# Optimization experiments

Measured on AMD Instinct MI355X. Metric: run time of the kernel, lower is better.

Reference implementation:

```python
import jax, jax.numpy as jnp
import numpy as np

INPUT_DIM = 512
LATENT_DIM = 64
H1, H2 = 128, 64  # hardcoded hidden widths in Encoder/Decoder
BATCH = 4096


def _xavier(key, shape):
    fan_out, fan_in = shape
    std = jnp.sqrt(2.0 / (fan_in + fan_out))
    return std * jax.random.normal(key, shape, dtype=jnp.float32)


def setup_inputs() -> dict:
    key = jax.random.key(0)
    ks = jax.random.split(key, 10)
    d = LATENT_DIM
    n_pairs = d * (d - 1) // 2
    n_funcs = 1 + d + n_pairs  # bias + states + pairwise products
    inp = {
        "x": jax.random.normal(ks[0], (BATCH, INPUT_DIM), dtype=jnp.float32),
        "xdot": jax.random.normal(ks[1], (BATCH, INPUT_DIM), dtype=jnp.float32),
        # encoder weights (torch Linear layout: [out, in])
        "We1": _xavier(ks[2], (H1, INPUT_DIM)), "be1": jnp.zeros((H1,), jnp.float32),
        "We2": _xavier(ks[3], (H2, H1)),        "be2": jnp.zeros((H2,), jnp.float32),
        "We3": _xavier(ks[4], (d, H2)),         "be3": jnp.zeros((d,), jnp.float32),
        # decoder weights
        "Wd1": _xavier(ks[5], (H2, d)),         "bd1": jnp.zeros((H2,), jnp.float32),
        "Wd2": _xavier(ks[6], (H1, H2)),        "bd2": jnp.zeros((H1,), jnp.float32),
        "Wd3": _xavier(ks[7], (INPUT_DIM, H1)), "bd3": jnp.zeros((INPUT_DIM,), jnp.float32),
        "XI": jnp.ones((n_funcs, d), jnp.float32),
        "XI_mask": jnp.ones((n_funcs, d), jnp.float32),
    }
    return inp


def _mlp_with_jacobian(x, Ws, bs):
    """3-layer relu MLP; returns output and per-sample analytic Jacobian [B,out,in].
    Jacobian = diag(m3) W3 diag(m2) W2 diag(m1) W1 with relu masks m_l."""
    h = x
    J = None
    for W, b in zip(Ws, bs):
        h = h @ W.T + b                      # [B, out_l]
        m = (h > 0).astype(h.dtype)          # relu mask (grad 0 at 0, matching torch)
        h = jnp.maximum(h, 0)
        Wm = m[:, :, None] * W[None]         # [B, out_l, in_l]
        J = Wm if J is None else jnp.einsum('boh,bhi->boi', Wm, J)
    return h, J


def _sindy_library(z):
    B, d = z.shape
    iu, ju = np.triu_indices(d, k=1)
    ones = jnp.ones((B, 1), z.dtype)
    pairs = z[:, iu] * z[:, ju]              # [B, d(d-1)/2]
    return jnp.concatenate([ones, z, pairs], axis=1)


def reference(x, xdot, We1, be1, We2, be2, We3, be3,
              Wd1, bd1, Wd2, bd2, Wd3, bd3, XI, XI_mask):
    z, Jenc = _mlp_with_jacobian(x, (We1, We2, We3), (be1, be2, be3))
    dz_dt = jnp.einsum('bli,bi->bl', Jenc, xdot)
    xh, Jdec = _mlp_with_jacobian(z, (Wd1, Wd2, Wd3), (bd1, bd2, bd3))
    theta = _sindy_library(z)
    dz_dt_sindy = theta @ (XI_mask * XI)
    dxh_dt = jnp.einsum('bol,bl->bo', Jdec, dz_dt_sindy)
    return (xh, dxh_dt, z, dz_dt, dz_dt_sindy)
```

## Files before the change

kernel.cpp:

```cpp
#include <hip/hip_runtime.h>

#define BATCH 4096
#define IN_DIM 512
#define H1DIM 128
#define H2DIM 64
#define DDIM 64
#define NFUNC 2081
#define NFPAD 2112
#define CHUNK 704
#define KS_PER_CHUNK 22

typedef short bf16x8 __attribute__((ext_vector_type(8)));
typedef float f32x4 __attribute__((ext_vector_type(4)));
#define MFMA(a,b,c) __builtin_amdgcn_mfma_f32_16x16x32_bf16(a,b,c,0,0,0)

#define WSZ1 (H1DIM*IN_DIM)
#define WSZ2 (H2DIM*H1DIM)
#define WSZ3 (DDIM*H2DIM)
#define WSZ4 (H2DIM*DDIM)
#define WSZ5 (H1DIM*H2DIM)
#define WSZ6 (IN_DIM*H1DIM)

__device__ __forceinline__ short f2b(float f) {
    union { float f; unsigned u; } x; x.f = f;
    unsigned r = x.u + 0x7fffu + ((x.u >> 16) & 1u);
    return (short)(r >> 16);
}
__device__ __forceinline__ float b2f(short s) {
    union { unsigned u; float f; } x; x.u = ((unsigned)(unsigned short)s) << 16;
    return x.f;
}
__device__ __forceinline__ void split3f(float v, short& s0, short& s1, short& s2) {
    s0 = f2b(v); float r = v - b2f(s0);
    s1 = f2b(r); float r2 = r - b2f(s1);
    s2 = f2b(r2);
}
__device__ __forceinline__ uint2 pk4(const short* s) {
    union { short s[4]; uint2 u; } z;
    z.s[0] = s[0]; z.s[1] = s[1]; z.s[2] = s[2]; z.s[3] = s[3];
    return z.u;
}

template<int N> __device__ __forceinline__ void waitv() {
    asm volatile("s_waitcnt vmcnt(%0)" :: "n"(N) : "memory");
    __builtin_amdgcn_sched_barrier(0);
}

__device__ __forceinline__ void st_b16(short* t, int RS, int r, int c, short v) {
    int b = (c * 2) ^ ((r & 7) << 4);
    *(short*)((char*)(t + r * RS) + b) = v;
}
__device__ __forceinline__ void st_b64(short* t, int RS, int r, int c0, uint2 v) {
    int b = (c0 * 2) ^ ((r & 7) << 4);
    *(uint2*)((char*)(t + r * RS) + b) = v;
}
__device__ __forceinline__ bf16x8 ld_af(const short* t, int RS, int lane, int kbase) {
    int r = lane & 15;
    int b = ((kbase + (lane >> 4) * 8) * 2) ^ ((r & 7) << 4);
    return *(const bf16x8*)((const char*)(t + r * RS) + b);
}
__device__ __forceinline__ bf16x8 ld_bp(const short* P, int blk, int lane) {
    return *(const bf16x8*)(P + ((size_t)blk * 64 + lane) * 8);
}

__device__ __forceinline__ void mf9(bf16x8 f0, bf16x8 f1, bf16x8 f2, bf16x8 fv,
                                    bf16x8 b0, bf16x8 b1, bf16x8 b2,
                                    f32x4& P, f32x4& Q, f32x4& V) {
    P = MFMA(f0, b0, P); Q = MFMA(f1, b1, Q);
    P = MFMA(f1, b0, P); Q = MFMA(f0, b1, Q);
    P = MFMA(f2, b0, P); Q = MFMA(f2, b1, Q);
    P = MFMA(f0, b2, P); Q = MFMA(f1, b2, Q);
    V = MFMA(fv, b0, V);
}

__device__ __forceinline__ void epi_store(short* t0, short* t1, short* t2, short* tv, int RS,
                                          int lane, int col, const f32x4& P, const f32x4& Q,
                                          const f32x4& V, float bb)
{
    #pragma unroll
    for (int q = 0; q < 4; ++q) {
        int row = (lane >> 4) * 4 + q;
        float pre = P[q] + Q[q] + bb;
        float h = fmaxf(pre, 0.f);
        short s0, s1, s2;
        split3f(h, s0, s1, s2);
        st_b16(t0, RS, row, col, s0);
        st_b16(t1, RS, row, col, s1);
        st_b16(t2, RS, row, col, s2);
        st_b16(tv, RS, row, col, pre > 0.f ? f2b(V[q]) : (short)0);
    }
}

template<int K>
__device__ void pack_w(const float* __restrict__ W, short* __restrict__ dst, int NK,
                       int gid, int nthr)
{
    for (int i = gid; i < NK; i += nthr) {
        int c = i / K, k = i % K;
        int cb = c >> 4, ks = k >> 5;
        int L = (((k >> 3) & 3) << 4) | (c & 15);
        int j = k & 7;
        int idx = ((cb * (K / 32) + ks) * 64 + L) * 8 + j;
        short s0, s1, s2; split3f(W[i], s0, s1, s2);
        dst[idx] = s0; dst[idx + NK] = s1; dst[idx + 2 * NK] = s2;
    }
}

__global__ void initk(const float* __restrict__ x, const float* __restrict__ xdot,
                      const float* __restrict__ We1, const float* __restrict__ We2,
                      const float* __restrict__ We3, const float* __restrict__ Wd1,
                      const float* __restrict__ Wd2, const float* __restrict__ Wd3,
                      const float* __restrict__ XI, const float* __restrict__ XIm,
                      float* __restrict__ xh, float* __restrict__ dxh,
                      short* Wp1, short* Wp2, short* Wp3, short* Wp4, short* Wp5, short* Wp6,
                      short* xiP, int2* pk)
{
    int gid = blockIdx.x * blockDim.x + threadIdx.x;
    int nthr = gridDim.x * blockDim.x;

    for (int i = gid; i < (BATCH / 16) * 16 * 64; i += nthr) {
        int L = i & 63, ks = (i >> 6) & 15, rb = i >> 10;
        int row = rb * 16 + (L & 15);
        int k0 = ks * 32 + ((L >> 4) << 3);
        const float* px = &x[(size_t)row * IN_DIM + k0];
        const float* pd = &xdot[(size_t)row * IN_DIM + k0];
        union { short s[8]; bf16x8 v; } a0, a1, a2, dv;
        #pragma unroll
        for (int j = 0; j < 8; ++j) {
            split3f(px[j], a0.s[j], a1.s[j], a2.s[j]);
            dv.s[j] = f2b(pd[j]);
        }
        short* bx = (short*)(xh + (size_t)rb * 8192);
        short* bd = (short*)(dxh + (size_t)rb * 8192);
        int off = (ks * 64 + L) * 8;
        *(bf16x8*)(bx + off) = a0.v;
        *(bf16x8*)(bx + 8192 + off) = a1.v;
        *(bf16x8*)(bd + off) = a2.v;
        *(bf16x8*)(bd + 8192 + off) = dv.v;
    }

    pack_w<512>(We1, Wp1, WSZ1, gid, nthr);
    pack_w<128>(We2, Wp2, WSZ2, gid, nthr);
    pack_w<64>(We3, Wp3, WSZ3, gid, nthr);
    pack_w<64>(Wd1, Wp4, WSZ4, gid, nthr);
    pack_w<64>(Wd2, Wp5, WSZ5, gid, nthr);
    pack_w<128>(Wd3, Wp6, WSZ6, gid, nthr);

    for (int i = gid; i < 4 * 66 * 64; i += nthr) {
        int cb = i / (66 * 64);
        int r = i - cb * (66 * 64);
        int ks = r >> 6, L = r & 63;
        int col = cb * 16 + (L & 15);
        union { short s[8]; bf16x8 v; } w;
        #pragma unroll
        for (int j = 0; j < 8; ++j) {
            int f = ks * 32 + ((L >> 4) << 3) + j;
            float v = (f < NFUNC) ? XI[(size_t)f * DDIM + col] * XIm[(size_t)f * DDIM + col] : 0.f;
            w.s[j] = f2b(v);
        }
        *(bf16x8*)(xiP + (size_t)i * 8) = w.v;
    }

    for (int f = gid; f < NFPAD; f += nthr) {
        int a, b;
        if (f == 0) { a = 64; b = 64; }
        else if (f <= DDIM) { a = f - 1; b = 64; }
        else if (f < NFUNC) {
            int p = f - 1 - DDIM; int i2 = 0, cum = 0;
            while (cum + (63 - i2) <= p) { cum += 63 - i2; ++i2; }
            a = i2; b = i2 + 1 + (p - cum);
        } else { a = 65; b = 65; }
        pk[f] = make_int2(a, b);
    }
}

__global__ __launch_bounds__(256, 1)
void fused(const float* __restrict__ be1, const float* __restrict__ be2,
           const float* __restrict__ be3, const float* __restrict__ bd1,
           const float* __restrict__ bd2, const float* __restrict__ bd3,
           const short* __restrict__ Wp1, const short* __restrict__ Wp2,
           const short* __restrict__ Wp3, const short* __restrict__ Wp4,
           const short* __restrict__ Wp5, const short* __restrict__ Wp6,
           const short* __restrict__ xiP, const int2* __restrict__ pk,
           float* __restrict__ xh, float* __restrict__ dxh, float* __restrict__ zo,
           float* __restrict__ dz, float* __restrict__ dzs)
{
    __shared__ __align__(1024) char lds[122880];
#define GLL(gp, lo) __builtin_amdgcn_global_load_lds( \
        (const __attribute__((address_space(1))) unsigned int*)(gp), \
        (__attribute__((address_space(3))) unsigned int*)&lds[lo], 16, 0, 0)

    short* h1s0 = (short*)(lds + 0);
    short* h1s1 = (short*)(lds + 4096);
    short* h1s2 = (short*)(lds + 8192);
    short* v1   = (short*)(lds + 12288);
    short* h2s0 = (short*)(lds + 16384);
    short* h2s1 = (short*)(lds + 18432);
    short* h2s2 = (short*)(lds + 20480);
    short* v2   = (short*)(lds + 22528);
    short* th   = (short*)(lds + 0);
    short* g1s0 = (short*)(lds + 0);
    short* g1s1 = (short*)(lds + 2048);
    short* g1s2 = (short*)(lds + 4096);
    short* u1   = (short*)(lds + 6144);
    short* g2s0 = (short*)(lds + 8192);
    short* g2s1 = (short*)(lds + 12288);
    short* g2s2 = (short*)(lds + 16384);
    short* u2   = (short*)(lds + 20480);
    short* zb0  = (short*)(lds + 24576);
    short* zb1  = (short*)(lds + 26624);
    short* zb2  = (short*)(lds + 28672);
    short* dzsb = (short*)(lds + 30720);
    float* zf   = (float*)(lds + 32768);

    const int tid = threadIdx.x, lane = tid & 63, wave = tid >> 6;
    const int row0 = blockIdx.x * 16;
    const int c16 = lane & 15;
    const int lane16 = lane * 16;
    const int tr = tid & 15, tf44 = (tid >> 4) * 44;

    float bb1[2] = { be1[wave * 32 + c16], be1[wave * 32 + 16 + c16] };
    float bb2 = be2[wave * 16 + c16];
    float bb3 = be3[wave * 16 + c16];
    float bD1 = bd1[wave * 16 + c16];
    float bD2[2] = { bd2[wave * 32 + c16], bd2[wave * 32 + 16 + c16] };
    float bD3[8];
    #pragma unroll
    for (int i = 0; i < 8; ++i) bD3[i] = bd3[wave * 128 + i * 16 + c16];

    f32x4 P1[2] = {}, Q1[2] = {}, V1[2] = {};
    {
        const char* bxc = (const char*)(xh + (size_t)blockIdx.x * 8192);
        const char* bdc = (const char*)(dxh + (size_t)blockIdx.x * 8192);
        const char* w1ac = (const char*)Wp1;
        const char* w1bc = (const char*)(Wp1 + WSZ1);
        const char* w1cc = (const char*)(Wp1 + 2 * WSZ1);
#define SLOT1(d) (unsigned)(wave * 30720 + (d) * 10240)
#define ISS1(ks, d) { unsigned sb = SLOT1(d); \
        const char* ga = bxc + (ks) * 1024 + lane16; \
        GLL(ga, sb);            GLL(ga + 16384, sb + 1024); \
        const char* gd = bdc + (ks) * 1024 + lane16; \
        GLL(gd, sb + 2048);     GLL(gd + 16384, sb + 3072); \
        int bA = ((wave * 2) * 16 + (ks)) * 1024 + lane16; \
        int bB = ((wave * 2 + 1) * 16 + (ks)) * 1024 + lane16; \
        GLL(w1ac + bA, sb + 4096); GLL(w1bc + bA, sb + 5120); GLL(w1cc + bA, sb + 6144); \
        GLL(w1ac + bB, sb + 7168); GLL(w1bc + bB, sb + 8192); GLL(w1cc + bB, sb + 9216); }
#define STEP1(ks, WN) { waitv<WN>(); unsigned sb = SLOT1((ks) % 3); \
        bf16x8 f0  = *(const bf16x8*)&lds[sb + lane16]; \
        bf16x8 f1  = *(const bf16x8*)&lds[sb + 1024 + lane16]; \
        bf16x8 f2  = *(const bf16x8*)&lds[sb + 2048 + lane16]; \
        bf16x8 fv  = *(const bf16x8*)&lds[sb + 3072 + lane16]; \
        bf16x8 b00 = *(const bf16x8*)&lds[sb + 4096 + lane16]; \
        bf16x8 b01 = *(const bf16x8*)&lds[sb + 5120 + lane16]; \
        bf16x8 b02 = *(const bf16x8*)&lds[sb + 6144 + lane16]; \
        bf16x8 b10 = *(const bf16x8*)&lds[sb + 7168 + lane16]; \
        bf16x8 b11 = *(const bf16x8*)&lds[sb + 8192 + lane16]; \
        bf16x8 b12 = *(const bf16x8*)&lds[sb + 9216 + lane16]; \
        mf9(f0, f1, f2, fv, b00, b01, b02, P1[0], Q1[0], V1[0]); \
        mf9(f0, f1, f2, fv, b10, b11, b12, P1[1], Q1[1], V1[1]); \
        __builtin_amdgcn_sched_barrier(0); \
        if ((ks) + 3 < 16) ISS1((ks) + 3, (ks) % 3) }

        ISS1(0, 0) ISS1(1, 1) ISS1(2, 2)
        STEP1(0, 20)  STEP1(1, 20)  STEP1(2, 20)  STEP1(3, 20)
        STEP1(4, 20)  STEP1(5, 20)  STEP1(6, 20)  STEP1(7, 20)
        STEP1(8, 20)  STEP1(9, 20)  STEP1(10, 20) STEP1(11, 20)
        STEP1(12, 20) STEP1(13, 20) STEP1(14, 10) STEP1(15, 0)
#undef ISS1
#undef STEP1
#undef SLOT1
    }
    __syncthreads();
    #pragma unroll
    for (int nf = 0; nf < 2; ++nf) {
        int col = wave * 32 + nf * 16 + c16;
        epi_store(h1s0, h1s1, h1s2, v1, 128, lane, col, P1[nf], Q1[nf], V1[nf], bb1[nf]);
    }
    bf16x8 L2B[4][3];
    #pragma unroll
    for (int ks = 0; ks < 4; ++ks) {
        int blk = wave * 4 + ks;
        L2B[ks][0] = ld_bp(Wp2, blk, lane);
        L2B[ks][1] = ld_bp(Wp2 + WSZ2, blk, lane);
        L2B[ks][2] = ld_bp(Wp2 + 2 * WSZ2, blk, lane);
    }
    __syncthreads();

    bf16x8 L3B[2][3];
    {
        bf16x8 Aa[4][4];
        #pragma unroll
        for (int ks = 0; ks < 4; ++ks) {
            Aa[ks][0] = ld_af(h1s0, 128, lane, ks * 32);
            Aa[ks][1] = ld_af(h1s1, 128, lane, ks * 32);
            Aa[ks][2] = ld_af(h1s2, 128, lane, ks * 32);
            Aa[ks][3] = ld_af(v1, 128, lane, ks * 32);
        }
        #pragma unroll
        for (int ks = 0; ks < 2; ++ks) {
            int blk = wave * 2 + ks;
            L3B[ks][0] = ld_bp(Wp3, blk, lane);
            L3B[ks][1] = ld_bp(Wp3 + WSZ3, blk, lane);
            L3B[ks][2] = ld_bp(Wp3 + 2 * WSZ3, blk, lane);
        }
        f32x4 P = {}, Q = {}, V = {};
        #pragma unroll
        for (int ks = 0; ks < 4; ++ks)
            mf9(Aa[ks][0], Aa[ks][1], Aa[ks][2], Aa[ks][3], L2B[ks][0], L2B[ks][1], L2B[ks][2], P, Q, V);
        epi_store(h2s0, h2s1, h2s2, v2, 64, lane, wave * 16 + c16, P, Q, V, bb2);
    }
    __syncthreads();

    bf16x8 X[KS_PER_CHUNK];
    {
        bf16x8 Aa[2][4];
        #pragma unroll
        for (int ks = 0; ks < 2; ++ks) {
            Aa[ks][0] = ld_af(h2s0, 64, lane, ks * 32);
            Aa[ks][1] = ld_af(h2s1, 64, lane, ks * 32);
            Aa[ks][2] = ld_af(h2s2, 64, lane, ks * 32);
            Aa[ks][3] = ld_af(v2, 64, lane, ks * 32);
        }
        f32x4 P = {}, Q = {}, V = {};
        #pragma unroll
        for (int ks = 0; ks < 2; ++ks)
            mf9(Aa[ks][0], Aa[ks][1], Aa[ks][2], Aa[ks][3], L3B[ks][0], L3B[ks][1], L3B[ks][2], P, Q, V);
        #pragma unroll
        for (int kk = 0; kk < KS_PER_CHUNK; ++kk)
            X[kk] = ld_bp(xiP, wave * 66 + kk, lane);
        int col = wave * 16 + c16;
        #pragma unroll
        for (int q = 0; q < 4; ++q) {
            int row = (lane >> 4) * 4 + q;
            float pre = P[q] + Q[q] + bb3;
            float hz = fmaxf(pre, 0.f);
            float vz = pre > 0.f ? V[q] : 0.f;
            zf[row * 68 + col] = hz;
            short s0, s1, s2;
            split3f(hz, s0, s1, s2);
            st_b16(zb0, 64, row, col, s0);
            st_b16(zb1, 64, row, col, s1);
            st_b16(zb2, 64, row, col, s2);
            zo[(size_t)(row0 + row) * DDIM + col] = hz;
            dz[(size_t)(row0 + row) * DDIM + col] = vz;
        }
        if (tid < 32) { int r = tid & 15; zf[r * 68 + 64 + (tid >> 4)] = (tid >> 4) ? 0.f : 1.f; }
    }
    __syncthreads();

    f32x4 sa0 = {}, sa1 = {};
#define BUILD(ch) { _Pragma("unroll") for (int g = 0; g < 11; ++g) { \
        int fl = tf44 + g * 4, fg = (ch) * CHUNK + fl; \
        int4 qa = *(const int4*)&pk[fg]; int4 qb = *(const int4*)&pk[fg + 2]; \
        float t0 = zf[tr * 68 + qa.x] * zf[tr * 68 + qa.y]; \
        float t1 = zf[tr * 68 + qa.z] * zf[tr * 68 + qa.w]; \
        float t2 = zf[tr * 68 + qb.x] * zf[tr * 68 + qb.y]; \
        float t3 = zf[tr * 68 + qb.z] * zf[tr * 68 + qb.w]; \
        short arr[4] = { f2b(t0), f2b(t1), f2b(t2), f2b(t3) }; \
        st_b64(th, 704, tr, fl, pk4(arr)); } }
#define SMF() { _Pragma("unroll") for (int kk = 0; kk < KS_PER_CHUNK; ++kk) { \
        bf16x8 a = ld_af(th, 704, lane, kk * 32); \
        if (kk & 1) sa1 = MFMA(a, X[kk], sa1); else sa0 = MFMA(a, X[kk], sa0); } }
#define ISX(ch) { _Pragma("unroll") for (int kk = 0; kk < KS_PER_CHUNK; ++kk) \
        X[kk] = ld_bp(xiP, wave * 66 + (ch) * KS_PER_CHUNK + kk, lane); }

    BUILD(0)
    __syncthreads();
    SMF() ISX(1)
    __syncthreads();
    BUILD(1)
    __syncthreads();
    SMF() ISX(2)
    __syncthreads();
    BUILD(2)
    __syncthreads();
    SMF()
#undef BUILD
#undef SMF
#undef ISX
    bf16x8 D1B[2][3];
    {
        f32x4 sacc = sa0 + sa1;
        #pragma unroll
        for (int ks = 0; ks < 2; ++ks) {
            int blk = wave * 2 + ks;
            D1B[ks][0] = ld_bp(Wp4, blk, lane);
            D1B[ks][1] = ld_bp(Wp4 + WSZ4, blk, lane);
            D1B[ks][2] = ld_bp(Wp4 + 2 * WSZ4, blk, lane);
        }
        int col = wave * 16 + c16;
        #pragma unroll
        for (int q = 0; q < 4; ++q) {
            int row = (lane >> 4) * 4 + q;
            float v = sacc[q];
            dzs[(size_t)(row0 + row) * DDIM + col] = v;
            st_b16(dzsb, 64, row, col, f2b(v));
        }
    }
    __syncthreads();

    bf16x8 D2B[4][3];
    {
        bf16x8 Aa[2][4];
        #pragma unroll
        for (int ks = 0; ks < 2; ++ks) {
            Aa[ks][0] = ld_af(zb0, 64, lane, ks * 32);
            Aa[ks][1] = ld_af(zb1, 64, lane, ks * 32);
            Aa[ks][2] = ld_af(zb2, 64, lane, ks * 32);
            Aa[ks][3] = ld_af(dzsb, 64, lane, ks * 32);
        }
        #pragma unroll
        for (int cf = 0; cf < 2; ++cf)
            #pragma unroll
            for (int ks = 0; ks < 2; ++ks) {
                int blk = (wave * 2 + cf) * 2 + ks;
                D2B[cf * 2 + ks][0] = ld_bp(Wp5, blk, lane);
                D2B[cf * 2 + ks][1] = ld_bp(Wp5 + WSZ5, blk, lane);
                D2B[cf * 2 + ks][2] = ld_bp(Wp5 + 2 * WSZ5, blk, lane);
            }
        f32x4 P = {}, Q = {}, V = {};
        #pragma unroll
        for (int ks = 0; ks < 2; ++ks)
            mf9(Aa[ks][0], Aa[ks][1], Aa[ks][2], Aa[ks][3], D1B[ks][0], D1B[ks][1], D1B[ks][2], P, Q, V);
        epi_store(g1s0, g1s1, g1s2, u1, 64, lane, wave * 16 + c16, P, Q, V, bD1);
    }
    __syncthreads();

    {
        bf16x8 Aa[2][4];
        #pragma unroll
        for (int ks = 0; ks < 2; ++ks) {
            Aa[ks][0] = ld_af(g1s0, 64, lane, ks * 32);
            Aa[ks][1] = ld_af(g1s1, 64, lane, ks * 32);
            Aa[ks][2] = ld_af(g1s2, 64, lane, ks * 32);
            Aa[ks][3] = ld_af(u1, 64, lane, ks * 32);
        }
        f32x4 P[2] = {}, Q[2] = {}, V[2] = {};
        #pragma unroll
        for (int cf = 0; cf < 2; ++cf)
            #pragma unroll
            for (int ks = 0; ks < 2; ++ks)
                mf9(Aa[ks][0], Aa[ks][1], Aa[ks][2], Aa[ks][3],
                    D2B[cf * 2 + ks][0], D2B[cf * 2 + ks][1], D2B[cf * 2 + ks][2],
                    P[cf], Q[cf], V[cf]);
        #pragma unroll
        for (int cf = 0; cf < 2; ++cf) {
            int col = wave * 32 + cf * 16 + c16;
            epi_store(g2s0, g2s1, g2s2, u2, 128, lane, col, P[cf], Q[cf], V[cf], bD2[cf]);
        }
    }
    __syncthreads();

    bf16x8 Ax0, Ax1, Ax2, Axv;
    const char* w6ac = (const char*)Wp6;
    const char* w6bc = (const char*)(Wp6 + WSZ6);
    const char* w6cc = (const char*)(Wp6 + 2 * WSZ6);
#define D3SLOT(d) (unsigned)(40960 + wave * 12288 + (d) * 3072)
#define D3ISS(h, s) { unsigned sb = D3SLOT((s) & 3); \
        int bo = ((wave * 8 + (h) * 4 + ((s) & 3)) * 4 + ((s) >> 2)) * 1024 + lane16; \
        GLL(w6ac + bo, sb); GLL(w6bc + bo, sb + 1024); GLL(w6cc + bo, sb + 2048); }
#define D3STEP(h, s, WN, Pa, Qa, Va) { waitv<WN>(); \
        if (((s) & 3) == 0) { int ks = (s) >> 2; \
            Ax0 = ld_af(g2s0, 128, lane, ks * 32); Ax1 = ld_af(g2s1, 128, lane, ks * 32); \
            Ax2 = ld_af(g2s2, 128, lane, ks * 32); Axv = ld_af(u2, 128, lane, ks * 32); } \
        { unsigned sb = D3SLOT((s) & 3); \
          bf16x8 c0 = *(const bf16x8*)&lds[sb + lane16]; \
          bf16x8 c1 = *(const bf16x8*)&lds[sb + 1024 + lane16]; \
          bf16x8 c2 = *(const bf16x8*)&lds[sb + 2048 + lane16]; \
          mf9(Ax0, Ax1, Ax2, Axv, c0, c1, c2, Pa[(s) & 3], Qa[(s) & 3], Va[(s) & 3]); } \
        __builtin_amdgcn_sched_barrier(0); \
        if ((s) + 4 < 16) D3ISS(h, (s) + 4) }
#define D3EPI(h, P_, Q_, V_) { _Pragma("unroll") for (int cf = 0; cf < 4; ++cf) { \
        int col = wave * 128 + (h) * 64 + cf * 16 + c16; \
        float bb = bD3[(h) * 4 + cf]; \
        _Pragma("unroll") for (int q = 0; q < 4; ++q) { \
            int row = (lane >> 4) * 4 + q; \
            float pre = P_[cf][q] + Q_[cf][q] + bb; \
            xh[(size_t)(row0 + row) * IN_DIM + col] = fmaxf(pre, 0.f); \
            dxh[(size_t)(row0 + row) * IN_DIM + col] = pre > 0.f ? V_[cf][q] : 0.f; } } }

    {
        f32x4 P[4] = {}, Q[4] = {}, V[4] = {};
        D3ISS(0, 0) D3ISS(0, 1) D3ISS(0, 2) D3ISS(0, 3)
        D3STEP(0, 0, 9, P, Q, V)  D3STEP(0, 1, 9, P, Q, V)  D3STEP(0, 2, 9, P, Q, V)  D3STEP(0, 3, 9, P, Q, V)
        D3STEP(0, 4, 9, P, Q, V)  D3STEP(0, 5, 9, P, Q, V)  D3STEP(0, 6, 9, P, Q, V)  D3STEP(0, 7, 9, P, Q, V)
        D3STEP(0, 8, 9, P, Q, V)  D3STEP(0, 9, 9, P, Q, V)  D3STEP(0, 10, 9, P, Q, V) D3STEP(0, 11, 9, P, Q, V)
        D3STEP(0, 12, 9, P, Q, V) D3STEP(0, 13, 6, P, Q, V) D3STEP(0, 14, 3, P, Q, V) D3STEP(0, 15, 0, P, Q, V)
        D3EPI(0, P, Q, V)
    }
    {
        f32x4 P[4] = {}, Q[4] = {}, V[4] = {};
        D3ISS(1, 0) D3ISS(1, 1) D3ISS(1, 2) D3ISS(1, 3)
        D3STEP(1, 0, 9, P, Q, V)  D3STEP(1, 1, 9, P, Q, V)  D3STEP(1, 2, 9, P, Q, V)  D3STEP(1, 3, 9, P, Q, V)
        D3STEP(1, 4, 9, P, Q, V)  D3STEP(1, 5, 9, P, Q, V)  D3STEP(1, 6, 9, P, Q, V)  D3STEP(1, 7, 9, P, Q, V)
        D3STEP(1, 8, 9, P, Q, V)  D3STEP(1, 9, 9, P, Q, V)  D3STEP(1, 10, 9, P, Q, V) D3STEP(1, 11, 9, P, Q, V)
        D3STEP(1, 12, 9, P, Q, V) D3STEP(1, 13, 6, P, Q, V) D3STEP(1, 14, 3, P, Q, V) D3STEP(1, 15, 0, P, Q, V)
        D3EPI(1, P, Q, V)
    }
#undef D3ISS
#undef D3STEP
#undef D3EPI
#undef D3SLOT
#undef GLL
}

extern "C" void kernel_launch(void* const* d_in, const int* in_sizes, int n_in,
                              void* d_out, int out_size, void* d_ws, size_t ws_size,
                              hipStream_t stream)
{
    const float* x    = (const float*)d_in[0];
    const float* xdot = (const float*)d_in[1];
    const float* We1  = (const float*)d_in[2];
    const float* be1  = (const float*)d_in[3];
    const float* We2  = (const float*)d_in[4];
    const float* be2  = (const float*)d_in[5];
    const float* We3  = (const float*)d_in[6];
    const float* be3  = (const float*)d_in[7];
    const float* Wd1  = (const float*)d_in[8];
    const float* bd1  = (const float*)d_in[9];
    const float* Wd2  = (const float*)d_in[10];
    const float* bd2  = (const float*)d_in[11];
    const float* Wd3  = (const float*)d_in[12];
    const float* bd3  = (const float*)d_in[13];
    const float* XI   = (const float*)d_in[14];
    const float* XIm  = (const float*)d_in[15];

    float* out = (float*)d_out;
    float* xh  = out;
    float* dxh = out + (size_t)BATCH * IN_DIM;
    float* zo  = dxh + (size_t)BATCH * IN_DIM;
    float* dz  = zo + (size_t)BATCH * DDIM;
    float* dzs = dz + (size_t)BATCH * DDIM;

    int2*  pk  = (int2*)d_ws;
    short* Wp1 = (short*)(pk + NFPAD);
    short* Wp2 = Wp1 + 3 * WSZ1;
    short* Wp3 = Wp2 + 3 * WSZ2;
    short* Wp4 = Wp3 + 3 * WSZ3;
    short* Wp5 = Wp4 + 3 * WSZ4;
    short* Wp6 = Wp5 + 3 * WSZ5;
    short* xiP = Wp6 + 3 * WSZ6;

    initk<<<1024, 256, 0, stream>>>(x, xdot, We1, We2, We3, Wd1, Wd2, Wd3, XI, XIm,
                                    xh, dxh, Wp1, Wp2, Wp3, Wp4, Wp5, Wp6, xiP, pk);
    fused<<<BATCH / 16, 256, 0, stream>>>(be1, be2, be3, bd1, bd2, bd3,
                                          Wp1, Wp2, Wp3, Wp4, Wp5, Wp6, xiP, pk,
                                          xh, dxh, zo, dz, dzs);
}
```

Measured before the change: 48.65 us.

## Pack two 16-row groups per 512-thread block with shallower pipelines

Each block now has 512 threads split into two independent quads of four waves, and each quad handles its own 16 batch rows in a private LDS region. The grid is halved and LDS grows to 160 KB. The layer-1 global-to-LDS pipeline drops from three to two stages and the decoder-output pipeline from four to three so both quads fit. This aims to raise waves per CU and latency hiding, but the shallower prefetch may expose memory latency, and block-wide __syncthreads now couple the two quads.

Result: slower. 66.16 us (+36.0%).

```diff
diff --git a/kernel.cpp b/kernel.cpp
--- a/kernel.cpp
+++ b/kernel.cpp
@@ -174,7 +174,7 @@
     }
 }
 
-__global__ __launch_bounds__(256, 1)
+__global__ __launch_bounds__(512)
 void fused(const float* __restrict__ be1, const float* __restrict__ be2,
            const float* __restrict__ be3, const float* __restrict__ bd1,
            const float* __restrict__ bd2, const float* __restrict__ bd3,
@@ -185,67 +185,70 @@
            float* __restrict__ xh, float* __restrict__ dxh, float* __restrict__ zo,
            float* __restrict__ dz, float* __restrict__ dzs)
 {
-    __shared__ __align__(1024) char lds[122880];
+    __shared__ __align__(1024) char lds[163840];
 #define GLL(gp, lo) __builtin_amdgcn_global_load_lds( \
         (const __attribute__((address_space(1))) unsigned int*)(gp), \
         (__attribute__((address_space(3))) unsigned int*)&lds[lo], 16, 0, 0)
 
-    short* h1s0 = (short*)(lds + 0);
-    short* h1s1 = (short*)(lds + 4096);
-    short* h1s2 = (short*)(lds + 8192);
-    short* v1   = (short*)(lds + 12288);
-    short* h2s0 = (short*)(lds + 16384);
-    short* h2s1 = (short*)(lds + 18432);
-    short* h2s2 = (short*)(lds + 20480);
-    short* v2   = (short*)(lds + 22528);
-    short* th   = (short*)(lds + 0);
-    short* g1s0 = (short*)(lds + 0);
-    short* g1s1 = (short*)(lds + 2048);
-    short* g1s2 = (short*)(lds + 4096);
-    short* u1   = (short*)(lds + 6144);
-    short* g2s0 = (short*)(lds + 8192);
-    short* g2s1 = (short*)(lds + 12288);
-    short* g2s2 = (short*)(lds + 16384);
-    short* u2   = (short*)(lds + 20480);
-    short* zb0  = (short*)(lds + 24576);
-    short* zb1  = (short*)(lds + 26624);
-    short* zb2  = (short*)(lds + 28672);
-    short* dzsb = (short*)(lds + 30720);
-    float* zf   = (float*)(lds + 32768);
-
     const int tid = threadIdx.x, lane = tid & 63, wave = tid >> 6;
-    const int row0 = blockIdx.x * 16;
+    const int wq = wave & 3, quad = wave >> 2;
+    const int qtid = tid & 255;
+    const int row0 = blockIdx.x * 32 + quad * 16;
     const int c16 = lane & 15;
     const int lane16 = lane * 16;
-    const int tr = tid & 15, tf44 = (tid >> 4) * 44;
-
-    float bb1[2] = { be1[wave * 32 + c16], be1[wave * 32 + 16 + c16] };
-    float bb2 = be2[wave * 16 + c16];
-    float bb3 = be3[wave * 16 + c16];
-    float bD1 = bd1[wave * 16 + c16];
-    float bD2[2] = { bd2[wave * 32 + c16], bd2[wave * 32 + 16 + c16] };
+    const int tr = qtid & 15, tf44 = (qtid >> 4) * 44;
+
+    char* Qb = lds + quad * 37120;
+    short* h1s0 = (short*)(Qb + 0);
+    short* h1s1 = (short*)(Qb + 4096);
+    short* h1s2 = (short*)(Qb + 8192);
+    short* v1   = (short*)(Qb + 12288);
+    short* h2s0 = (short*)(Qb + 16384);
+    short* h2s1 = (short*)(Qb + 18432);
+    short* h2s2 = (short*)(Qb + 20480);
+    short* v2   = (short*)(Qb + 22528);
+    short* th   = (short*)(Qb + 0);
+    short* g1s0 = (short*)(Qb + 0);
+    short* g1s1 = (short*)(Qb + 2048);
+    short* g1s2 = (short*)(Qb + 4096);
+    short* u1   = (short*)(Qb + 6144);
+    short* g2s0 = (short*)(Qb + 8192);
+    short* g2s1 = (short*)(Qb + 12288);
+    short* g2s2 = (short*)(Qb + 16384);
+    short* u2   = (short*)(Qb + 20480);
+    short* zb0  = (short*)(Qb + 24576);
+    short* zb1  = (short*)(Qb + 26624);
+    short* zb2  = (short*)(Qb + 28672);
+    short* dzsb = (short*)(Qb + 30720);
+    float* zf   = (float*)(Qb + 32768);
+
+    float bb1[2] = { be1[wq * 32 + c16], be1[wq * 32 + 16 + c16] };
+    float bb2 = be2[wq * 16 + c16];
+    float bb3 = be3[wq * 16 + c16];
+    float bD1 = bd1[wq * 16 + c16];
+    float bD2[2] = { bd2[wq * 32 + c16], bd2[wq * 32 + 16 + c16] };
     float bD3[8];
     #pragma unroll
-    for (int i = 0; i < 8; ++i) bD3[i] = bd3[wave * 128 + i * 16 + c16];
+    for (int i = 0; i < 8; ++i) bD3[i] = bd3[wq * 128 + i * 16 + c16];
 
     f32x4 P1[2] = {}, Q1[2] = {}, V1[2] = {};
     {
-        const char* bxc = (const char*)(xh + (size_t)blockIdx.x * 8192);
-        const char* bdc = (const char*)(dxh + (size_t)blockIdx.x * 8192);
+        const char* bxc = (const char*)(xh + ((size_t)blockIdx.x * 2 + quad) * 8192);
+        const char* bdc = (const char*)(dxh + ((size_t)blockIdx.x * 2 + quad) * 8192);
         const char* w1ac = (const char*)Wp1;
         const char* w1bc = (const char*)(Wp1 + WSZ1);
         const char* w1cc = (const char*)(Wp1 + 2 * WSZ1);
-#define SLOT1(d) (unsigned)(wave * 30720 + (d) * 10240)
+#define SLOT1(d) (unsigned)(wave * 20480 + (d) * 10240)
 #define ISS1(ks, d) { unsigned sb = SLOT1(d); \
         const char* ga = bxc + (ks) * 1024 + lane16; \
         GLL(ga, sb);            GLL(ga + 16384, sb + 1024); \
         const char* gd = bdc + (ks) * 1024 + lane16; \
         GLL(gd, sb + 2048);     GLL(gd + 16384, sb + 3072); \
-        int bA = ((wave * 2) * 16 + (ks)) * 1024 + lane16; \
-        int bB = ((wave * 2 + 1) * 16 + (ks)) * 1024 + lane16; \
+        int bA = ((wq * 2) * 16 + (ks)) * 1024 + lane16; \
+        int bB = ((wq * 2 + 1) * 16 + (ks)) * 1024 + lane16; \
         GLL(w1ac + bA, sb + 4096); GLL(w1bc + bA, sb + 5120); GLL(w1cc + bA, sb + 6144); \
         GLL(w1ac + bB, sb + 7168); GLL(w1bc + bB, sb + 8192); GLL(w1cc + bB, sb + 9216); }
-#define STEP1(ks, WN) { waitv<WN>(); unsigned sb = SLOT1((ks) % 3); \
+#define STEP1(ks, WN) { waitv<WN>(); unsigned sb = SLOT1((ks) & 1); \
         bf16x8 f0  = *(const bf16x8*)&lds[sb + lane16]; \
         bf16x8 f1  = *(const bf16x8*)&lds[sb + 1024 + lane16]; \
         bf16x8 f2  = *(const bf16x8*)&lds[sb + 2048 + lane16]; \
@@ -259,13 +262,13 @@
         mf9(f0, f1, f2, fv, b00, b01, b02, P1[0], Q1[0], V1[0]); \
         mf9(f0, f1, f2, fv, b10, b11, b12, P1[1], Q1[1], V1[1]); \
         __builtin_amdgcn_sched_barrier(0); \
-        if ((ks) + 3 < 16) ISS1((ks) + 3, (ks) % 3) }
-
-        ISS1(0, 0) ISS1(1, 1) ISS1(2, 2)
-        STEP1(0, 20)  STEP1(1, 20)  STEP1(2, 20)  STEP1(3, 20)
-        STEP1(4, 20)  STEP1(5, 20)  STEP1(6, 20)  STEP1(7, 20)
-        STEP1(8, 20)  STEP1(9, 20)  STEP1(10, 20) STEP1(11, 20)
-        STEP1(12, 20) STEP1(13, 20) STEP1(14, 10) STEP1(15, 0)
+        if ((ks) + 2 < 16) ISS1((ks) + 2, (ks) & 1) }
+
+        ISS1(0, 0) ISS1(1, 1)
+        STEP1(0, 10)  STEP1(1, 10)  STEP1(2, 10)  STEP1(3, 10)
+        STEP1(4, 10)  STEP1(5, 10)  STEP1(6, 10)  STEP1(7, 10)
+        STEP1(8, 10)  STEP1(9, 10)  STEP1(10, 10) STEP1(11, 10)
+        STEP1(12, 10) STEP1(13, 10) STEP1(14, 10) STEP1(15, 0)
 #undef ISS1
 #undef STEP1
 #undef SLOT1
@@ -273,13 +276,13 @@
     __syncthreads();
     #pragma unroll
     for (int nf = 0; nf < 2; ++nf) {
-        int col = wave * 32 + nf * 16 + c16;
+        int col = wq * 32 + nf * 16 + c16;
         epi_store(h1s0, h1s1, h1s2, v1, 128, lane, col, P1[nf], Q1[nf], V1[nf], bb1[nf]);
     }
     bf16x8 L2B[4][3];
     #pragma unroll
     for (int ks = 0; ks < 4; ++ks) {
-        int blk = wave * 4 + ks;
+        int blk = wq * 4 + ks;
         L2B[ks][0] = ld_bp(Wp2, blk, lane);
         L2B[ks][1] = ld_bp(Wp2 + WSZ2, blk, lane);
         L2B[ks][2] = ld_bp(Wp2 + 2 * WSZ2, blk, lane);
@@ -298,7 +301,7 @@
         }
         #pragma unroll
         for (int ks = 0; ks < 2; ++ks) {
-            int blk = wave * 2 + ks;
+            int blk = wq * 2 + ks;
             L3B[ks][0] = ld_bp(Wp3, blk, lane);
             L3B[ks][1] = ld_bp(Wp3 + WSZ3, blk, lane);
             L3B[ks][2] = ld_bp(Wp3 + 2 * WSZ3, blk, lane);
@@ -307,7 +310,7 @@
         #pragma unroll
         for (int ks = 0; ks < 4; ++ks)
             mf9(Aa[ks][0], Aa[ks][1], Aa[ks][2], Aa[ks][3], L2B[ks][0], L2B[ks][1], L2B[ks][2], P, Q, V);
-        epi_store(h2s0, h2s1, h2s2, v2, 64, lane, wave * 16 + c16, P, Q, V, bb2);
+        epi_store(h2s0, h2s1, h2s2, v2, 64, lane, wq * 16 + c16, P, Q, V, bb2);
     }
     __syncthreads();
 
@@ -327,8 +330,8 @@
             mf9(Aa[ks][0], Aa[ks][1], Aa[ks][2], Aa[ks][3], L3B[ks][0], L3B[ks][1], L3B[ks][2], P, Q, V);
         #pragma unroll
         for (int kk = 0; kk < KS_PER_CHUNK; ++kk)
-            X[kk] = ld_bp(xiP, wave * 66 + kk, lane);
-        int col = wave * 16 + c16;
+            X[kk] = ld_bp(xiP, wq * 66 + kk, lane);
+        int col = wq * 16 + c16;
         #pragma unroll
         for (int q = 0; q < 4; ++q) {
             int row = (lane >> 4) * 4 + q;
@@ -344,7 +347,7 @@
             zo[(size_t)(row0 + row) * DDIM + col] = hz;
             dz[(size_t)(row0 + row) * DDIM + col] = vz;
         }
-        if (tid < 32) { int r = tid & 15; zf[r * 68 + 64 + (tid >> 4)] = (tid >> 4) ? 0.f : 1.f; }
+        if (qtid < 32) { int r = qtid & 15; zf[r * 68 + 64 + (qtid >> 4)] = (qtid >> 4) ? 0.f : 1.f; }
     }
     __syncthreads();
 
@@ -362,7 +365,7 @@
         bf16x8 a = ld_af(th, 704, lane, kk * 32); \
         if (kk & 1) sa1 = MFMA(a, X[kk], sa1); else sa0 = MFMA(a, X[kk], sa0); } }
 #define ISX(ch) { _Pragma("unroll") for (int kk = 0; kk < KS_PER_CHUNK; ++kk) \
-        X[kk] = ld_bp(xiP, wave * 66 + (ch) * KS_PER_CHUNK + kk, lane); }
+        X[kk] = ld_bp(xiP, wq * 66 + (ch) * KS_PER_CHUNK + kk, lane); }
 
     BUILD(0)
     __syncthreads();
@@ -383,12 +386,12 @@
         f32x4 sacc = sa0 + sa1;
         #pragma unroll
         for (int ks = 0; ks < 2; ++ks) {
-            int blk = wave * 2 + ks;
+            int blk = wq * 2 + ks;
             D1B[ks][0] = ld_bp(Wp4, blk, lane);
             D1B[ks][1] = ld_bp(Wp4 + WSZ4, blk, lane);
             D1B[ks][2] = ld_bp(Wp4 + 2 * WSZ4, blk, lane);
         }
-        int col = wave * 16 + c16;
+        int col = wq * 16 + c16;
         #pragma unroll
         for (int q = 0; q < 4; ++q) {
             int row = (lane >> 4) * 4 + q;
@@ -413,7 +416,7 @@
         for (int cf = 0; cf < 2; ++cf)
             #pragma unroll
             for (int ks = 0; ks < 2; ++ks) {
-                int blk = (wave * 2 + cf) * 2 + ks;
+                int blk = (wq * 2 + cf) * 2 + ks;
                 D2B[cf * 2 + ks][0] = ld_bp(Wp5, blk, lane);
                 D2B[cf * 2 + ks][1] = ld_bp(Wp5 + WSZ5, blk, lane);
                 D2B[cf * 2 + ks][2] = ld_bp(Wp5 + 2 * WSZ5, blk, lane);
@@ -422,7 +425,7 @@
         #pragma unroll
         for (int ks = 0; ks < 2; ++ks)
             mf9(Aa[ks][0], Aa[ks][1], Aa[ks][2], Aa[ks][3], D1B[ks][0], D1B[ks][1], D1B[ks][2], P, Q, V);
-        epi_store(g1s0, g1s1, g1s2, u1, 64, lane, wave * 16 + c16, P, Q, V, bD1);
+        epi_store(g1s0, g1s1, g1s2, u1, 64, lane, wq * 16 + c16, P, Q, V, bD1);
     }
     __syncthreads();
 
@@ -445,7 +448,7 @@
                     P[cf], Q[cf], V[cf]);
         #pragma unroll
         for (int cf = 0; cf < 2; ++cf) {
-            int col = wave * 32 + cf * 16 + c16;
+            int col = wq * 32 + cf * 16 + c16;
             epi_store(g2s0, g2s1, g2s2, u2, 128, lane, col, P[cf], Q[cf], V[cf], bD2[cf]);
         }
     }
@@ -455,23 +458,23 @@
     const char* w6ac = (const char*)Wp6;
     const char* w6bc = (const char*)(Wp6 + WSZ6);
     const char* w6cc = (const char*)(Wp6 + 2 * WSZ6);
-#define D3SLOT(d) (unsigned)(40960 + wave * 12288 + (d) * 3072)
-#define D3ISS(h, s) { unsigned sb = D3SLOT((s) & 3); \
-        int bo = ((wave * 8 + (h) * 4 + ((s) & 3)) * 4 + ((s) >> 2)) * 1024 + lane16; \
+#define D3SLOT(d) (unsigned)(74240 + wave * 9216 + (d) * 3072)
+#define D3ISS(h, s) { unsigned sb = D3SLOT((s) % 3); \
+        int bo = ((wq * 8 + (h) * 4 + ((s) & 3)) * 4 + ((s) >> 2)) * 1024 + lane16; \
         GLL(w6ac + bo, sb); GLL(w6bc + bo, sb + 1024); GLL(w6cc + bo, sb + 2048); }
 #define D3STEP(h, s, WN, Pa, Qa, Va) { waitv<WN>(); \
         if (((s) & 3) == 0) { int ks = (s) >> 2; \
             Ax0 = ld_af(g2s0, 128, lane, ks * 32); Ax1 = ld_af(g2s1, 128, lane, ks * 32); \
             Ax2 = ld_af(g2s2, 128, lane, ks * 32); Axv = ld_af(u2, 128, lane, ks * 32); } \
-        { unsigned sb = D3SLOT((s) & 3); \
+        { unsigned sb = D3SLOT((s) % 3); \
           bf16x8 c0 = *(const bf16x8*)&lds[sb + lane16]; \
           bf16x8 c1 = *(const bf16x8*)&lds[sb + 1024 + lane16]; \
           bf16x8 c2 = *(const bf16x8*)&lds[sb + 2048 + lane16]; \
           mf9(Ax0, Ax1, Ax2, Axv, c0, c1, c2, Pa[(s) & 3], Qa[(s) & 3], Va[(s) & 3]); } \
         __builtin_amdgcn_sched_barrier(0); \
-        if ((s) + 4 < 16) D3ISS(h, (s) + 4) }
+        if ((s) + 3 < 16) D3ISS(h, (s) + 3) }
 #define D3EPI(h, P_, Q_, V_) { _Pragma("unroll") for (int cf = 0; cf < 4; ++cf) { \
-        int col = wave * 128 + (h) * 64 + cf * 16 + c16; \
+        int col = wq * 128 + (h) * 64 + cf * 16 + c16; \
         float bb = bD3[(h) * 4 + cf]; \
         _Pragma("unroll") for (int q = 0; q < 4; ++q) { \
             int row = (lane >> 4) * 4 + q; \
@@ -481,20 +484,20 @@
 
     {
         f32x4 P[4] = {}, Q[4] = {}, V[4] = {};
-        D3ISS(0, 0) D3ISS(0, 1) D3ISS(0, 2) D3ISS(0, 3)
-        D3STEP(0, 0, 9, P, Q, V)  D3STEP(0, 1, 9, P, Q, V)  D3STEP(0, 2, 9, P, Q, V)  D3STEP(0, 3, 9, P, Q, V)
-        D3STEP(0, 4, 9, P, Q, V)  D3STEP(0, 5, 9, P, Q, V)  D3STEP(0, 6, 9, P, Q, V)  D3STEP(0, 7, 9, P, Q, V)
-        D3STEP(0, 8, 9, P, Q, V)  D3STEP(0, 9, 9, P, Q, V)  D3STEP(0, 10, 9, P, Q, V) D3STEP(0, 11, 9, P, Q, V)
-        D3STEP(0, 12, 9, P, Q, V) D3STEP(0, 13, 6, P, Q, V) D3STEP(0, 14, 3, P, Q, V) D3STEP(0, 15, 0, P, Q, V)
+        D3ISS(0, 0) D3ISS(0, 1) D3ISS(0, 2)
+        D3STEP(0, 0, 6, P, Q, V)  D3STEP(0, 1, 6, P, Q, V)  D3STEP(0, 2, 6, P, Q, V)  D3STEP(0, 3, 6, P, Q, V)
+        D3STEP(0, 4, 6, P, Q, V)  D3STEP(0, 5, 6, P, Q, V)  D3STEP(0, 6, 6, P, Q, V)  D3STEP(0, 7, 6, P, Q, V)
+        D3STEP(0, 8, 6, P, Q, V)  D3STEP(0, 9, 6, P, Q, V)  D3STEP(0, 10, 6, P, Q, V) D3STEP(0, 11, 6, P, Q, V)
+        D3STEP(0, 12, 6, P, Q, V) D3STEP(0, 13, 6, P, Q, V) D3STEP(0, 14, 3, P, Q, V) D3STEP(0, 15, 0, P, Q, V)
         D3EPI(0, P, Q, V)
     }
     {
         f32x4 P[4] = {}, Q[4] = {}, V[4] = {};
-        D3ISS(1, 0) D3ISS(1, 1) D3ISS(1, 2) D3ISS(1, 3)
-        D3STEP(1, 0, 9, P, Q, V)  D3STEP(1, 1, 9, P, Q, V)  D3STEP(1, 2, 9, P, Q, V)  D3STEP(1, 3, 9, P, Q, V)
-        D3STEP(1, 4, 9, P, Q, V)  D3STEP(1, 5, 9, P, Q, V)  D3STEP(1, 6, 9, P, Q, V)  D3STEP(1, 7, 9, P, Q, V)
-        D3STEP(1, 8, 9, P, Q, V)  D3STEP(1, 9, 9, P, Q, V)  D3STEP(1, 10, 9, P, Q, V) D3STEP(1, 11, 9, P, Q, V)
-        D3STEP(1, 12, 9, P, Q, V) D3STEP(1, 13, 6, P, Q, V) D3STEP(1, 14, 3, P, Q, V) D3STEP(1, 15, 0, P, Q, V)
+        D3ISS(1, 0) D3ISS(1, 1) D3ISS(1, 2)
+        D3STEP(1, 0, 6, P, Q, V)  D3STEP(1, 1, 6, P, Q, V)  D3STEP(1, 2, 6, P, Q, V)  D3STEP(1, 3, 6, P, Q, V)
+        D3STEP(1, 4, 6, P, Q, V)  D3STEP(1, 5, 6, P, Q, V)  D3STEP(1, 6, 6, P, Q, V)  D3STEP(1, 7, 6, P, Q, V)
+        D3STEP(1, 8, 6, P, Q, V)  D3STEP(1, 9, 6, P, Q, V)  D3STEP(1, 10, 6, P, Q, V) D3STEP(1, 11, 6, P, Q, V)
+        D3STEP(1, 12, 6, P, Q, V) D3STEP(1, 13, 6, P, Q, V) D3STEP(1, 14, 3, P, Q, V) D3STEP(1, 15, 0, P, Q, V)
         D3EPI(1, P, Q, V)
     }
 #undef D3ISS
@@ -543,7 +546,7 @@
 
     initk<<<1024, 256, 0, stream>>>(x, xdot, We1, We2, We3, Wd1, Wd2, Wd3, XI, XIm,
                                     xh, dxh, Wp1, Wp2, Wp3, Wp4, Wp5, Wp6, xiP, pk);
-    fused<<<BATCH / 16, 256, 0, stream>>>(be1, be2, be3, bd1, bd2, bd3,
+    fused<<<BATCH / 32, 512, 0, stream>>>(be1, be2, be3, bd1, bd2, bd3,
                                           Wp1, Wp2, Wp3, Wp4, Wp5, Wp6, xiP, pk,
                                           xh, dxh, zo, dz, dzs);
 }
```
